# Performance work log

Measured on AMD Instinct MI355X. Metric: run time of the kernel, lower is better.

## Reference

```python
import jax, jax.numpy as jnp
import numpy as np

BN_EPS = 1e-5

def _conv1x1(x, W, b):
    # x: (B,C,H,W), W: (O,C) -> (B,O,H,W)
    return jnp.einsum('oc,bchw->bohw', W, x) + b[None, :, None, None]

def setup_inputs() -> dict:
    key = jax.random.key(0)
    ks = jax.random.split(key, 6)
    B, C, H, W = 4, 256, 64, 64
    cq = C // 8
    x  = jax.random.normal(ks[0], (B, C, H, W), jnp.float32)
    Wq = jax.random.normal(ks[1], (cq, C), jnp.float32) * (1.0 / np.sqrt(C))
    Wk = jax.random.normal(ks[2], (cq, C), jnp.float32) * (1.0 / np.sqrt(C))
    Wv = jax.random.normal(ks[3], (C, C), jnp.float32) * (1.0 / np.sqrt(C))
    Wo = jax.random.normal(ks[4], (C, C, 3, 3), jnp.float32) * (1.0 / np.sqrt(C * 9))
    return {
        'x': x,
        'Wq': Wq, 'bq': jnp.zeros((cq,), jnp.float32),
        'Wk': Wk, 'bk': jnp.zeros((cq,), jnp.float32),
        'Wv': Wv, 'bv': jnp.zeros((C,), jnp.float32),
        'Wo': Wo, 'bo': jnp.zeros((C,), jnp.float32),
        'bn_gamma': jnp.ones((C,), jnp.float32),
        'bn_beta':  jnp.zeros((C,), jnp.float32),
        'bn_mean':  jnp.zeros((C,), jnp.float32),
        'bn_var':   jnp.ones((C,), jnp.float32),
    }

def reference(x, Wq, bq, Wk, bk, Wv, bv, Wo, bo, bn_gamma, bn_beta, bn_mean, bn_var):
    B, C, H, W = x.shape
    cq = Wq.shape[0]
    N = H * W
    q = _conv1x1(x, Wq, bq).reshape(B, cq, N)   # (B,cq,N)
    k = _conv1x1(x, Wk, bk).reshape(B, cq, N)   # (B,cq,N)
    v = _conv1x1(x, Wv, bv).reshape(B, C, N)    # (B,C,N)
    scale = cq ** (-0.5)
    attn = jnp.einsum('bcn,bcm->bnm', q, k) * scale   # (B,N,N)
    attn = jax.nn.softmax(attn, axis=-1)
    out = jnp.einsum('bnm,bcm->bcn', attn, v).reshape(B, C, H, W)
    # conv_output: 3x3 conv + BN (inference stats) + ReLU
    out = jax.lax.conv_general_dilated(
        out, Wo, window_strides=(1, 1), padding=((1, 1), (1, 1)),
        dimension_numbers=('NCHW', 'OIHW', 'NCHW')) + bo[None, :, None, None]
    inv = bn_gamma * jax.lax.rsqrt(bn_var + BN_EPS)
    out = out * inv[None, :, None, None] + (bn_beta - bn_mean * inv)[None, :, None, None]
    out = jax.nn.relu(out)
    return out + x
```

## Files before the change

### kernel.cpp

```cpp
#include <hip/hip_runtime.h>
#include <hip/hip_bf16.h>
#include <math.h>

#define N_TOK 4096

typedef __attribute__((ext_vector_type(8))) short short8;
typedef __attribute__((ext_vector_type(4))) float f32x4;

#define MFMA16(a, b, c) __builtin_amdgcn_mfma_f32_16x16x32_bf16(a, b, c, 0, 0, 0)

__device__ inline unsigned pack_bf16x2(float a, float b) {
    __hip_bfloat16 ha = __float2bfloat16(a), hb = __float2bfloat16(b);
    unsigned short ua = *(unsigned short*)&ha, ub = *(unsigned short*)&hb;
    return (unsigned)ua | ((unsigned)ub << 16);
}

__device__ inline float bf2f(unsigned short u) {
    unsigned v = ((unsigned)u) << 16;
    union { unsigned u; float f; } cv; cv.u = v; return cv.f;
}

__device__ inline int swz4(int h, int row) { return (h ^ row ^ (row >> 2)) & 3; }

__global__ __launch_bounds__(256) void xt_prep_kernel(
    const float* __restrict__ x, __hip_bfloat16* __restrict__ xt)
{
    __shared__ __hip_bfloat16 tl[64][72];
    int blk = blockIdx.x;
    int cg = blk & 3, ng = (blk >> 2) & 63, b = blk >> 8;
    int n0 = ng * 64, c0 = cg * 64;
    int t = threadIdx.x;
    int cr = t >> 4, part = t & 15;
#pragma unroll
    for (int rep = 0; rep < 4; ++rep) {
        int c = rep * 16 + cr;
        float4 v4 = *(const float4*)&x[((size_t)(b * 256 + c0 + c)) * N_TOK + n0 + part * 4];
        tl[part * 4 + 0][c] = __float2bfloat16(v4.x);
        tl[part * 4 + 1][c] = __float2bfloat16(v4.y);
        tl[part * 4 + 2][c] = __float2bfloat16(v4.z);
        tl[part * 4 + 3][c] = __float2bfloat16(v4.w);
    }
    __syncthreads();
    int n = t >> 2, g = t & 3;
    uint4 u0 = *(uint4*)&tl[n][g * 16];
    uint4 u1 = *(uint4*)&tl[n][g * 16 + 8];
    __hip_bfloat16* dst = &xt[((size_t)(b * N_TOK + n0 + n)) * 256 + c0 + g * 16];
    *(uint4*)dst = u0;
    *(uint4*)&dst[8] = u1;
}

__global__ __launch_bounds__(256) void w_prep_kernel(
    const float* __restrict__ Wo, const float* __restrict__ Wq,
    const float* __restrict__ Wk, const float* __restrict__ Wv,
    __hip_bfloat16* __restrict__ Wt, __hip_bfloat16* __restrict__ Wqk,
    __hip_bfloat16* __restrict__ Wvb)
{
    int blk = blockIdx.x, t = threadIdx.x;
    if (blk < 256) {
        const float* src = &Wo[(size_t)(blk * 256 + t) * 9];
#pragma unroll
        for (int tap = 0; tap < 9; ++tap)
            Wt[(size_t)(tap * 256 + blk) * 256 + t] = __float2bfloat16(src[tap]);
    } else if (blk < 260) {
        int r0 = (blk - 256) * 64;
        for (int r = r0; r < r0 + 64; ++r)
            Wvb[r * 256 + t] = __float2bfloat16(Wv[r * 256 + t]);
    } else {
        for (int r = 0; r < 32; ++r) {
            Wqk[r * 256 + t]        = __float2bfloat16(Wq[r * 256 + t]);
            Wqk[(r + 32) * 256 + t] = __float2bfloat16(Wk[r * 256 + t]);
        }
    }
}

__global__ __launch_bounds__(256) void qk_mfma_kernel(
    const __hip_bfloat16* __restrict__ xt, const __hip_bfloat16* __restrict__ Wqk,
    const float* __restrict__ bq, const float* __restrict__ bk,
    __hip_bfloat16* __restrict__ qg, __hip_bfloat16* __restrict__ kg)
{
    int blk = blockIdx.x;
    int b = blk >> 6, n0 = (blk & 63) * 64;
    int t = threadIdx.x, w = t >> 6, lane = t & 63;
    int l15 = lane & 15, l4 = lane >> 4;
    int n = n0 + w * 16 + l15;

    f32x4 zf = {0.f, 0.f, 0.f, 0.f};
    f32x4 acc[4];
#pragma unroll
    for (int m = 0; m < 4; ++m) acc[m] = zf;

    const __hip_bfloat16* xrow = &xt[((size_t)(b * N_TOK + n)) * 256];
    for (int k0 = 0; k0 < 256; k0 += 32) {
        short8 bfr = *(const short8*)&xrow[k0 + l4 * 8];
#pragma unroll
        for (int m = 0; m < 4; ++m) {
            short8 af = *(const short8*)&Wqk[(size_t)(m * 16 + l15) * 256 + k0 + l4 * 8];
            acc[m] = MFMA16(af, bfr, acc[m]);
        }
    }
    f32x4 bq0 = *(const f32x4*)&bq[l4 * 4];
    f32x4 bq1 = *(const f32x4*)&bq[16 + l4 * 4];
    f32x4 bk0 = *(const f32x4*)&bk[l4 * 4];
    f32x4 bk1 = *(const f32x4*)&bk[16 + l4 * 4];
    size_t obase = (size_t)(b * N_TOK + n) * 32;
    uint2 u;
    u.x = pack_bf16x2(acc[0][0] + bq0[0], acc[0][1] + bq0[1]);
    u.y = pack_bf16x2(acc[0][2] + bq0[2], acc[0][3] + bq0[3]);
    *(uint2*)&qg[obase + l4 * 4] = u;
    u.x = pack_bf16x2(acc[1][0] + bq1[0], acc[1][1] + bq1[1]);
    u.y = pack_bf16x2(acc[1][2] + bq1[2], acc[1][3] + bq1[3]);
    *(uint2*)&qg[obase + 16 + l4 * 4] = u;
    u.x = pack_bf16x2(acc[2][0] + bk0[0], acc[2][1] + bk0[1]);
    u.y = pack_bf16x2(acc[2][2] + bk0[2], acc[2][3] + bk0[3]);
    *(uint2*)&kg[obase + l4 * 4] = u;
    u.x = pack_bf16x2(acc[3][0] + bk1[0], acc[3][1] + bk1[1]);
    u.y = pack_bf16x2(acc[3][2] + bk1[2], acc[3][3] + bk1[3]);
    *(uint2*)&kg[obase + 16 + l4 * 4] = u;
}

__global__ __launch_bounds__(256) void v_mfma_kernel(
    const __hip_bfloat16* __restrict__ xt, const __hip_bfloat16* __restrict__ Wvb,
    const float* __restrict__ bv, __hip_bfloat16* __restrict__ vg)
{
    int blk = blockIdx.x;
    int b = blk >> 7, ch = (blk >> 6) & 1, n0 = (blk & 63) * 64;
    int c0 = ch * 128;
    int t = threadIdx.x, w = t >> 6, lane = t & 63;
    int l15 = lane & 15, l4 = lane >> 4;
    int n = n0 + w * 16 + l15;

    f32x4 zf = {0.f, 0.f, 0.f, 0.f};
    f32x4 acc[8];
#pragma unroll
    for (int m = 0; m < 8; ++m) acc[m] = zf;

    const __hip_bfloat16* xrow = &xt[((size_t)(b * N_TOK + n)) * 256];
    for (int k0 = 0; k0 < 256; k0 += 32) {
        short8 bfr = *(const short8*)&xrow[k0 + l4 * 8];
#pragma unroll
        for (int m = 0; m < 8; ++m) {
            short8 af = *(const short8*)&Wvb[(size_t)(c0 + m * 16 + l15) * 256 + k0 + l4 * 8];
            acc[m] = MFMA16(af, bfr, acc[m]);
        }
    }
#pragma unroll
    for (int m = 0; m < 8; ++m) {
        int cb = c0 + m * 16 + l4 * 4;
        f32x4 bvv = *(const f32x4*)&bv[cb];
#pragma unroll
        for (int r = 0; r < 4; ++r)
            vg[((size_t)(b * 256 + cb + r)) * N_TOK + n] = __float2bfloat16(acc[m][r] + bvv[r]);
    }
}

__global__ __launch_bounds__(256, 4) void flash_kernel(
    const __hip_bfloat16* __restrict__ qg, const __hip_bfloat16* __restrict__ kg,
    const __hip_bfloat16* __restrict__ vg,
    __hip_bfloat16* __restrict__ ph0, __hip_bfloat16* __restrict__ ph1,
    float* __restrict__ Lh)
{
    __shared__ __hip_bfloat16 v_lds[2][128 * 64];
    __shared__ __hip_bfloat16 p_lds[4][16 * 64];

    int blk = blockIdx.x;
    int work = (blk & 7) * 128 + (blk >> 3);
    int g = work >> 7;
    int kh = g >> 2, cs = (g >> 1) & 1, bl = g & 1;
    int rem = work & 127;
    int b = ((rem >> 6) << 1) | bl;
    int qb = rem & 63;
    int n0 = qb * 64;
    int t = threadIdx.x, w = t >> 6, lane = t & 63;
    int l15 = lane & 15, l4 = lane >> 4;
    const float SC = 0.17677669529663687f * 1.4426950408889634f;
    const float SHIFT = 8.0f * 1.4426950408889634f;

    short8 qf = *(const short8*)&qg[((size_t)(b * N_TOK + n0 + w * 16 + l15)) * 32 + l4 * 8];

    f32x4 zf = {0.f, 0.f, 0.f, 0.f};
    f32x4 acc[8];
#pragma unroll
    for (int ct = 0; ct < 8; ++ct) acc[ct] = zf;
    float Lr0 = 0.f, Lr1 = 0.f;

    int c = t >> 1;
    int kb4 = (t & 1) * 4;

    const __hip_bfloat16* vrow = &vg[((size_t)(b * 256 + cs * 128 + c)) * N_TOK + kh * 2048];
    const __hip_bfloat16* kbase = &kg[((size_t)(b * N_TOK + kh * 2048)) * 32];

    uint4 vp[4];
    short8 kfr[4], kfn[4];

#pragma unroll
    for (int j = 0; j < 4; ++j)
        vp[j] = *(const uint4*)&vrow[(kb4 + j) * 8];
#pragma unroll
    for (int kt = 0; kt < 4; ++kt)
        kfr[kt] = *(const short8*)&kbase[(kt * 16 + l15) * 32 + l4 * 8];
#pragma unroll
    for (int j = 0; j < 4; ++j)
        *(uint4*)&v_lds[0][c * 64 + (((2 * (kb4 + j)) ^ (c & 14)) << 2)] = vp[j];
    __syncthreads();

    int buf = 0;
    for (int it = 0; it < 32; ++it) {
        int nm0 = it * 64 + 64;
        bool more = (it < 31);
        if (more) {
#pragma unroll
            for (int j = 0; j < 4; ++j)
                vp[j] = *(const uint4*)&vrow[nm0 + (kb4 + j) * 8];
#pragma unroll
            for (int kt = 0; kt < 4; ++kt)
                kfn[kt] = *(const short8*)&kbase[(size_t)(nm0 + kt * 16 + l15) * 32 + l4 * 8];
        }

        f32x4 sf[4];
#pragma unroll
        for (int kt = 0; kt < 4; ++kt) sf[kt] = MFMA16(kfr[kt], qf, zf);

        float pm[16];
#pragma unroll
        for (int kt = 0; kt < 4; ++kt) {
#pragma unroll
            for (int r = 0; r < 4; ++r)
                pm[kt * 4 + r] = exp2f(sf[kt][r] * SC - SHIFT);
            float s01 = pm[kt * 4 + 0] + pm[kt * 4 + 1];
            float s23 = pm[kt * 4 + 2] + pm[kt * 4 + 3];
            if (kt & 1) Lr1 += s01 + s23; else Lr0 += s01 + s23;
        }

#pragma unroll
        for (int kt = 0; kt < 4; ++kt) {
            uint2 u;
            u.x = pack_bf16x2(pm[kt * 4 + 0], pm[kt * 4 + 1]);
            u.y = pack_bf16x2(pm[kt * 4 + 2], pm[kt * 4 + 3]);
            *(uint2*)&p_lds[w][l15 * 64 + (((kt * 4 + l4) ^ (l15 & 14)) << 2)] = u;
        }
        short8 pb[2];
#pragma unroll
        for (int ks = 0; ks < 2; ++ks)
            pb[ks] = *(const short8*)&p_lds[w][l15 * 64 + (((ks * 8 + l4 * 2) ^ (l15 & 14)) << 2)];

#pragma unroll
        for (int ct = 0; ct < 8; ++ct) {
            int cr = ct * 16 + l15;
#pragma unroll
            for (int ks = 0; ks < 2; ++ks) {
                short8 vf = *(const short8*)&v_lds[buf][cr * 64 + (((ks * 8 + l4 * 2) ^ (cr & 14)) << 2)];
                acc[ct] = MFMA16(vf, pb[ks], acc[ct]);
            }
        }

        if (more) {
#pragma unroll
            for (int j = 0; j < 4; ++j)
                *(uint4*)&v_lds[buf ^ 1][c * 64 + (((2 * (kb4 + j)) ^ (c & 14)) << 2)] = vp[j];
#pragma unroll
            for (int kt = 0; kt < 4; ++kt) kfr[kt] = kfn[kt];
            buf ^= 1;
        }
        __syncthreads();
    }

    float Lr = Lr0 + Lr1;
    Lr += __shfl_xor(Lr, 16);
    Lr += __shfl_xor(Lr, 32);

    int nq = n0 + w * 16 + l15;
    if (cs == 0 && l4 == 0)
        Lh[kh * 16384 + b * 4096 + nq] = Lr;

    __hip_bfloat16* pdst = kh ? ph1 : ph0;
    size_t pix = (size_t)(b * N_TOK + nq);
#pragma unroll
    for (int ct = 0; ct < 8; ++ct) {
        int cl = cs * 128 + ct * 16 + l4 * 4;
        uint2 u;
        u.x = pack_bf16x2(acc[ct][0], acc[ct][1]);
        u.y = pack_bf16x2(acc[ct][2], acc[ct][3]);
        *(uint2*)&pdst[pix * 256 + cl] = u;
    }
}

__global__ __launch_bounds__(256) void linv_kernel(
    const float* __restrict__ Lh, float* __restrict__ Linv)
{
    int i = blockIdx.x * 256 + threadIdx.x;
    Linv[i] = 1.f / (Lh[i] + Lh[16384 + i]);
}

__global__ __launch_bounds__(256) void conv_mfma_kernel(
    const __hip_bfloat16* __restrict__ ph0, const __hip_bfloat16* __restrict__ ph1,
    const float* __restrict__ Linv, const __hip_bfloat16* __restrict__ Wt,
    const float* __restrict__ bo,  const float* __restrict__ gamma,
    const float* __restrict__ beta, const float* __restrict__ mean,
    const float* __restrict__ var, const float* __restrict__ x,
    float* __restrict__ out)
{
    __shared__ __hip_bfloat16 in_lds[324 * 32];
    __shared__ __hip_bfloat16 wt_lds[9 * 64 * 32];

    int blk = blockIdx.x;
    int sp = blk & 15, ob = (blk >> 4) & 3, b = blk >> 6;
    int y0 = (sp >> 2) * 16, x0 = (sp & 3) * 16;
    int o0 = ob * 64;
    int t = threadIdx.x;
    int w = t >> 6, lane = t & 63;
    int l15 = lane & 15, l4 = lane >> 4;

    f32x4 zf = {0.f, 0.f, 0.f, 0.f};
    f32x4 acc[4][4];
#pragma unroll
    for (int m = 0; m < 4; ++m)
#pragma unroll
        for (int n = 0; n < 4; ++n) acc[m][n] = zf;

    for (int cc = 0; cc < 256; cc += 32) {
        __syncthreads();
        for (int jj = t; jj < 1296; jj += 256) {
            int pix = jj >> 2, h = jj & 3;
            int iy = pix / 18, ix = pix - iy * 18;
            int gy = y0 - 1 + iy, gx = x0 - 1 + ix;
            uint4 val = {0u, 0u, 0u, 0u};
            if (gy >= 0 && gy < 64 && gx >= 0 && gx < 64) {
                int bn = b * 4096 + gy * 64 + gx;
                float inv = Linv[bn];
                size_t e = (size_t)bn * 256 + cc + h * 8;
                uint4 a  = *(const uint4*)&ph0[e];
                uint4 b4 = *(const uint4*)&ph1[e];
                const unsigned* ap = (const unsigned*)&a;
                const unsigned* bp = (const unsigned*)&b4;
                unsigned* vpn = (unsigned*)&val;
#pragma unroll
                for (int j = 0; j < 4; ++j) {
                    float lo = (bf2f((unsigned short)(ap[j] & 0xffff)) +
                                bf2f((unsigned short)(bp[j] & 0xffff))) * inv;
                    float hi = (bf2f((unsigned short)(ap[j] >> 16)) +
                                bf2f((unsigned short)(bp[j] >> 16))) * inv;
                    vpn[j] = pack_bf16x2(lo, hi);
                }
            }
            *(uint4*)&in_lds[pix * 32 + swz4(h, pix) * 8] = val;
        }
        for (int jj = t; jj < 2304; jj += 256) {
            int tap = jj >> 8, rem = jj & 255;
            int o = rem >> 2, h = rem & 3;
            uint4 wv = *(const uint4*)&Wt[((size_t)(tap * 256 + o0 + o)) * 256 + cc + h * 8];
            *(uint4*)&wt_lds[tap * 2048 + o * 32 + swz4(h, o) * 8] = wv;
        }
        __syncthreads();

#pragma unroll
        for (int ky = 0; ky < 3; ++ky) {
#pragma unroll
            for (int kx = 0; kx < 3; ++kx) {
                int tap = ky * 3 + kx;
                short8 af[4];
#pragma unroll
                for (int m = 0; m < 4; ++m) {
                    int orow = m * 16 + l15;
                    af[m] = *(const short8*)&wt_lds[tap * 2048 + orow * 32 + swz4(l4, orow) * 8];
                }
#pragma unroll
                for (int ntw = 0; ntw < 4; ++ntw) {
                    int yy = w * 4 + ntw;
                    int p = (yy + ky) * 18 + kx + l15;
                    short8 bfr = *(const short8*)&in_lds[p * 32 + swz4(l4, p) * 8];
#pragma unroll
                    for (int m = 0; m < 4; ++m)
                        acc[m][ntw] = MFMA16(af[m], bfr, acc[m][ntw]);
                }
            }
        }
    }

#pragma unroll
    for (int m = 0; m < 4; ++m) {
#pragma unroll
        for (int r = 0; r < 4; ++r) {
            int oc = o0 + m * 16 + l4 * 4 + r;
            float inv = gamma[oc] * rsqrtf(var[oc] + 1e-5f);
            float sh  = (bo[oc] - mean[oc]) * inv + beta[oc];
#pragma unroll
            for (int ntw = 0; ntw < 4; ++ntw) {
                int gy = y0 + w * 4 + ntw, gx = x0 + l15;
                size_t idx = (size_t)(b * 256 + oc) * 4096 + (size_t)gy * 64 + gx;
                float yv = acc[m][ntw][r] * inv + sh;
                yv = fmaxf(yv, 0.f);
                out[idx] = yv + x[idx];
            }
        }
    }
}

extern "C" void kernel_launch(void* const* d_in, const int* in_sizes, int n_in,
                              void* d_out, int out_size, void* d_ws, size_t ws_size,
                              hipStream_t stream)
{
    const float* x  = (const float*)d_in[0];
    const float* Wq = (const float*)d_in[1];
    const float* bq = (const float*)d_in[2];
    const float* Wk = (const float*)d_in[3];
    const float* bk = (const float*)d_in[4];
    const float* Wv = (const float*)d_in[5];
    const float* bv = (const float*)d_in[6];
    const float* Wo = (const float*)d_in[7];
    const float* bo = (const float*)d_in[8];
    const float* gm = (const float*)d_in[9];
    const float* bt = (const float*)d_in[10];
    const float* mn = (const float*)d_in[11];
    const float* vr = (const float*)d_in[12];
    float* out = (float*)d_out;

    char* wsb = (char*)d_ws;
    __hip_bfloat16* qg  = (__hip_bfloat16*)(wsb);
    __hip_bfloat16* kg  = (__hip_bfloat16*)(wsb + (1u  << 20));
    __hip_bfloat16* vg  = (__hip_bfloat16*)(wsb + (2u  << 20));
    __hip_bfloat16* att = (__hip_bfloat16*)(wsb + (10u << 20));
    __hip_bfloat16* Wt  = (__hip_bfloat16*)(wsb + (18u << 20));
    __hip_bfloat16* xt  = (__hip_bfloat16*)(wsb + (20u << 20));
    __hip_bfloat16* Wqk = (__hip_bfloat16*)(wsb + (28u << 20));
    __hip_bfloat16* Wvb = (__hip_bfloat16*)(wsb + (28u << 20) + 65536);
    float*          Lh  = (float*)(wsb + (28u << 20) + 262144);
    float*          Linv= (float*)(wsb + (28u << 20) + 393216);

    __hip_bfloat16* ph0 = xt;
    __hip_bfloat16* ph1 = att;

    w_prep_kernel  <<<261,  256, 0, stream>>>(Wo, Wq, Wk, Wv, Wt, Wqk, Wvb);
    xt_prep_kernel <<<1024, 256, 0, stream>>>(x, xt);
    qk_mfma_kernel <<<256,  256, 0, stream>>>(xt, Wqk, bq, bk, qg, kg);
    v_mfma_kernel  <<<512,  256, 0, stream>>>(xt, Wvb, bv, vg);
    flash_kernel   <<<1024, 256, 0, stream>>>(qg, kg, vg, ph0, ph1, Lh);
    linv_kernel    <<<64,   256, 0, stream>>>(Lh, Linv);
    conv_mfma_kernel<<<256, 256, 0, stream>>>(ph0, ph1, Linv, Wt, bo, gm, bt, mn, vr, x, out);
}
```

Baseline: 171.1 us.

## Double query rows per wave in flash kernel and stage K through LDS

Each wave now handles 32 query rows instead of 16, so every V fragment read from LDS feeds two MFMAs, and the block count is halved. K tiles are loaded cooperatively into a double-buffered, swizzled LDS buffer instead of each wave fetching its own K fragments from global memory. The aim is to cut LDS and global traffic per unit of MFMA work. In exchange, register use doubles for accumulators, launch bounds drop to 2 blocks per CU, and fewer blocks means less parallelism to hide latency.

```diff
diff --git a/kernel.cpp b/kernel.cpp
--- a/kernel.cpp
+++ b/kernel.cpp
@@ -153,54 +153,60 @@
     }
 }
 
-__global__ __launch_bounds__(256, 4) void flash_kernel(
+__global__ __launch_bounds__(256, 2) void flash_kernel(
     const __hip_bfloat16* __restrict__ qg, const __hip_bfloat16* __restrict__ kg,
     const __hip_bfloat16* __restrict__ vg,
     __hip_bfloat16* __restrict__ ph0, __hip_bfloat16* __restrict__ ph1,
     float* __restrict__ Lh)
 {
     __shared__ __hip_bfloat16 v_lds[2][128 * 64];
-    __shared__ __hip_bfloat16 p_lds[4][16 * 64];
+    __shared__ __hip_bfloat16 k_lds[2][64 * 32];
+    __shared__ __hip_bfloat16 p_lds[4][32 * 64];
 
     int blk = blockIdx.x;
-    int work = (blk & 7) * 128 + (blk >> 3);
-    int g = work >> 7;
+    int work = (blk & 7) * 64 + (blk >> 3);
+    int g = work >> 6;
     int kh = g >> 2, cs = (g >> 1) & 1, bl = g & 1;
-    int rem = work & 127;
-    int b = ((rem >> 6) << 1) | bl;
-    int qb = rem & 63;
-    int n0 = qb * 64;
+    int rem = work & 63;
+    int b = ((rem >> 5) << 1) | bl;
+    int qgp = rem & 31;
     int t = threadIdx.x, w = t >> 6, lane = t & 63;
     int l15 = lane & 15, l4 = lane >> 4;
+    int qw = qgp * 128 + w * 32;
     const float SC = 0.17677669529663687f * 1.4426950408889634f;
     const float SHIFT = 8.0f * 1.4426950408889634f;
 
-    short8 qf = *(const short8*)&qg[((size_t)(b * N_TOK + n0 + w * 16 + l15)) * 32 + l4 * 8];
+    short8 qf[2];
+#pragma unroll
+    for (int qs = 0; qs < 2; ++qs)
+        qf[qs] = *(const short8*)&qg[((size_t)(b * N_TOK + qw + qs * 16 + l15)) * 32 + l4 * 8];
 
     f32x4 zf = {0.f, 0.f, 0.f, 0.f};
-    f32x4 acc[8];
-#pragma unroll
-    for (int ct = 0; ct < 8; ++ct) acc[ct] = zf;
-    float Lr0 = 0.f, Lr1 = 0.f;
-
-    int c = t >> 1;
+    f32x4 acc[2][8];
+#pragma unroll
+    for (int qs = 0; qs < 2; ++qs)
+#pragma unroll
+        for (int ct = 0; ct < 8; ++ct) acc[qs][ct] = zf;
+    float Lr[2] = {0.f, 0.f};
+
+    int vc  = t >> 1;
     int kb4 = (t & 1) * 4;
-
-    const __hip_bfloat16* vrow = &vg[((size_t)(b * 256 + cs * 128 + c)) * N_TOK + kh * 2048];
+    int kr  = t >> 2;
+    int kch = t & 3;
+
+    const __hip_bfloat16* vrow  = &vg[((size_t)(b * 256 + cs * 128 + vc)) * N_TOK + kh * 2048];
     const __hip_bfloat16* kbase = &kg[((size_t)(b * N_TOK + kh * 2048)) * 32];
 
-    uint4 vp[4];
-    short8 kfr[4], kfn[4];
+    uint4 vp[4], kp;
 
 #pragma unroll
     for (int j = 0; j < 4; ++j)
         vp[j] = *(const uint4*)&vrow[(kb4 + j) * 8];
-#pragma unroll
-    for (int kt = 0; kt < 4; ++kt)
-        kfr[kt] = *(const short8*)&kbase[(kt * 16 + l15) * 32 + l4 * 8];
+    kp = *(const uint4*)&kbase[kr * 32 + kch * 8];
 #pragma unroll
     for (int j = 0; j < 4; ++j)
-        *(uint4*)&v_lds[0][c * 64 + (((2 * (kb4 + j)) ^ (c & 14)) << 2)] = vp[j];
+        *(uint4*)&v_lds[0][vc * 64 + (((2 * (kb4 + j)) ^ (vc & 14)) << 2)] = vp[j];
+    *(uint4*)&k_lds[0][kr * 32 + swz4(kch, kr) * 8] = kp;
     __syncthreads();
 
     int buf = 0;
@@ -211,76 +217,84 @@
 #pragma unroll
             for (int j = 0; j < 4; ++j)
                 vp[j] = *(const uint4*)&vrow[nm0 + (kb4 + j) * 8];
+            kp = *(const uint4*)&kbase[(size_t)(nm0 + kr) * 32 + kch * 8];
+        }
+
+        short8 kf[4];
+#pragma unroll
+        for (int kt = 0; kt < 4; ++kt) {
+            int row = kt * 16 + l15;
+            kf[kt] = *(const short8*)&k_lds[buf][row * 32 + swz4(l4, row) * 8];
+        }
+        f32x4 sf[2][4];
+#pragma unroll
+        for (int qs = 0; qs < 2; ++qs)
 #pragma unroll
             for (int kt = 0; kt < 4; ++kt)
-                kfn[kt] = *(const short8*)&kbase[(size_t)(nm0 + kt * 16 + l15) * 32 + l4 * 8];
-        }
-
-        f32x4 sf[4];
-#pragma unroll
-        for (int kt = 0; kt < 4; ++kt) sf[kt] = MFMA16(kfr[kt], qf, zf);
-
-        float pm[16];
-#pragma unroll
-        for (int kt = 0; kt < 4; ++kt) {
-#pragma unroll
-            for (int r = 0; r < 4; ++r)
-                pm[kt * 4 + r] = exp2f(sf[kt][r] * SC - SHIFT);
-            float s01 = pm[kt * 4 + 0] + pm[kt * 4 + 1];
-            float s23 = pm[kt * 4 + 2] + pm[kt * 4 + 3];
-            if (kt & 1) Lr1 += s01 + s23; else Lr0 += s01 + s23;
-        }
-
-#pragma unroll
-        for (int kt = 0; kt < 4; ++kt) {
+                sf[qs][kt] = MFMA16(kf[kt], qf[qs], zf);
+
+#pragma unroll
+        for (int qs = 0; qs < 2; ++qs) {
+            int prow = qs * 16 + l15;
+#pragma unroll
+            for (int kt = 0; kt < 4; ++kt) {
+                float p0 = exp2f(sf[qs][kt][0] * SC - SHIFT);
+                float p1 = exp2f(sf[qs][kt][1] * SC - SHIFT);
+                float p2 = exp2f(sf[qs][kt][2] * SC - SHIFT);
+                float p3 = exp2f(sf[qs][kt][3] * SC - SHIFT);
+                Lr[qs] += (p0 + p1) + (p2 + p3);
+                uint2 u;
+                u.x = pack_bf16x2(p0, p1);
+                u.y = pack_bf16x2(p2, p3);
+                *(uint2*)&p_lds[w][prow * 64 + (((kt * 4 + l4) ^ (l15 & 14)) << 2)] = u;
+            }
+        }
+
+#pragma unroll
+        for (int ks = 0; ks < 2; ++ks) {
+            short8 pb[2];
+#pragma unroll
+            for (int qs = 0; qs < 2; ++qs)
+                pb[qs] = *(const short8*)&p_lds[w][(qs * 16 + l15) * 64 +
+                         (((ks * 8 + l4 * 2) ^ (l15 & 14)) << 2)];
+#pragma unroll
+            for (int ct = 0; ct < 8; ++ct) {
+                int cr = ct * 16 + l15;
+                short8 vf = *(const short8*)&v_lds[buf][cr * 64 +
+                           (((ks * 8 + l4 * 2) ^ (cr & 14)) << 2)];
+                acc[0][ct] = MFMA16(vf, pb[0], acc[0][ct]);
+                acc[1][ct] = MFMA16(vf, pb[1], acc[1][ct]);
+            }
+        }
+
+        if (more) {
+#pragma unroll
+            for (int j = 0; j < 4; ++j)
+                *(uint4*)&v_lds[buf ^ 1][vc * 64 + (((2 * (kb4 + j)) ^ (vc & 14)) << 2)] = vp[j];
+            *(uint4*)&k_lds[buf ^ 1][kr * 32 + swz4(kch, kr) * 8] = kp;
+            buf ^= 1;
+        }
+        __syncthreads();
+    }
+
+#pragma unroll
+    for (int qs = 0; qs < 2; ++qs) {
+        float L = Lr[qs];
+        L += __shfl_xor(L, 16);
+        L += __shfl_xor(L, 32);
+        int nq = qw + qs * 16 + l15;
+        if (cs == 0 && l4 == 0)
+            Lh[kh * 16384 + b * 4096 + nq] = L;
+        __hip_bfloat16* pdst = kh ? ph1 : ph0;
+        size_t pix = (size_t)(b * N_TOK + nq);
+#pragma unroll
+        for (int ct = 0; ct < 8; ++ct) {
+            int cl = cs * 128 + ct * 16 + l4 * 4;
             uint2 u;
-            u.x = pack_bf16x2(pm[kt * 4 + 0], pm[kt * 4 + 1]);
-            u.y = pack_bf16x2(pm[kt * 4 + 2], pm[kt * 4 + 3]);
-            *(uint2*)&p_lds[w][l15 * 64 + (((kt * 4 + l4) ^ (l15 & 14)) << 2)] = u;
-        }
-        short8 pb[2];
-#pragma unroll
-        for (int ks = 0; ks < 2; ++ks)
-            pb[ks] = *(const short8*)&p_lds[w][l15 * 64 + (((ks * 8 + l4 * 2) ^ (l15 & 14)) << 2)];
-
-#pragma unroll
-        for (int ct = 0; ct < 8; ++ct) {
-            int cr = ct * 16 + l15;
-#pragma unroll
-            for (int ks = 0; ks < 2; ++ks) {
-                short8 vf = *(const short8*)&v_lds[buf][cr * 64 + (((ks * 8 + l4 * 2) ^ (cr & 14)) << 2)];
-                acc[ct] = MFMA16(vf, pb[ks], acc[ct]);
-            }
-        }
-
-        if (more) {
-#pragma unroll
-            for (int j = 0; j < 4; ++j)
-                *(uint4*)&v_lds[buf ^ 1][c * 64 + (((2 * (kb4 + j)) ^ (c & 14)) << 2)] = vp[j];
-#pragma unroll
-            for (int kt = 0; kt < 4; ++kt) kfr[kt] = kfn[kt];
-            buf ^= 1;
-        }
-        __syncthreads();
-    }
-
-    float Lr = Lr0 + Lr1;
-    Lr += __shfl_xor(Lr, 16);
-    Lr += __shfl_xor(Lr, 32);
-
-    int nq = n0 + w * 16 + l15;
-    if (cs == 0 && l4 == 0)
-        Lh[kh * 16384 + b * 4096 + nq] = Lr;
-
-    __hip_bfloat16* pdst = kh ? ph1 : ph0;
-    size_t pix = (size_t)(b * N_TOK + nq);
-#pragma unroll
-    for (int ct = 0; ct < 8; ++ct) {
-        int cl = cs * 128 + ct * 16 + l4 * 4;
-        uint2 u;
-        u.x = pack_bf16x2(acc[ct][0], acc[ct][1]);
-        u.y = pack_bf16x2(acc[ct][2], acc[ct][3]);
-        *(uint2*)&pdst[pix * 256 + cl] = u;
+            u.x = pack_bf16x2(acc[qs][ct][0], acc[qs][ct][1]);
+            u.y = pack_bf16x2(acc[qs][ct][2], acc[qs][ct][3]);
+            *(uint2*)&pdst[pix * 256 + cl] = u;
+        }
     }
 }
 
@@ -433,7 +447,7 @@
     xt_prep_kernel <<<1024, 256, 0, stream>>>(x, xt);
     qk_mfma_kernel <<<256,  256, 0, stream>>>(xt, Wqk, bq, bk, qg, kg);
     v_mfma_kernel  <<<512,  256, 0, stream>>>(xt, Wvb, bv, vg);
-    flash_kernel   <<<1024, 256, 0, stream>>>(qg, kg, vg, ph0, ph1, Lh);
+    flash_kernel   <<<512,  256, 0, stream>>>(qg, kg, vg, ph0, ph1, Lh);
     linv_kernel    <<<64,   256, 0, stream>>>(Lh, Linv);
     conv_mfma_kernel<<<256, 256, 0, stream>>>(ph0, ph1, Linv, Wt, bo, gm, bt, mn, vr, x, out);
 }
```

Result: no change. 168.9 us (-1.3%).
